# Kernel tuning notes

Measured on AMD Instinct MI355X. Metric: run time of the kernel, lower is better.

## Reference

```python
import jax, jax.numpy as jnp
import numpy as np

KAPPA = 0.1          # temperature for sinkhorn routing
SINK_ITERS = 3
SINK_EPS = 1e-6
NORM_EPS = 1e-12     # F.normalize clamp
LOG_EPS = 2.220446049250313e-16  # np.finfo(float).eps
K_TOP = 1


def _l2norm(v, axis=-1):
    n = jnp.sqrt(jnp.sum(v * v, axis=axis, keepdims=True))
    return v / jnp.maximum(n, NORM_EPS)


def _sinkhorn(log_alpha):
    # log_alpha: [K, N]
    L = jnp.exp(log_alpha)
    for _ in range(SINK_ITERS):
        L = L / (jnp.sum(L, axis=1, keepdims=True) + SINK_EPS)
        L = L / (jnp.sum(L, axis=0, keepdims=True) + SINK_EPS)
    return L


def setup_inputs() -> dict:
    key = jax.random.key(0)
    ks = jax.random.split(key, 16)
    dim = 1024
    N = 32768
    lora_dim = [8, 16, 32, 48, 64, 96, 128]
    inp = {
        "x": jax.random.normal(ks[0], (N, dim), dtype=jnp.float32),
        "prototypes": jax.random.normal(ks[1], (7, dim), dtype=jnp.float32),
    }
    for e, d in enumerate(lora_dim):
        # torch Linear weight: [out_features, in_features]
        inp[f"A{e}"] = jax.random.normal(ks[2 + 2 * e], (d, dim), dtype=jnp.float32) * (1.0 / np.sqrt(dim))
        inp[f"B{e}"] = jax.random.normal(ks[3 + 2 * e], (dim, d), dtype=jnp.float32) * (1.0 / np.sqrt(d))
    return inp


def reference(x, prototypes, A0, B0, A1, B1, A2, B2, A3, B3, A4, B4, A5, B5, A6, B6):
    A = [A0, A1, A2, A3, A4, A5, A6]
    B = [B0, B1, B2, B3, B4, B5, B6]
    N = x.shape[0]
    num_experts = len(A)

    # --- sinkhorn routing: gates [N, K] ---
    x_n = _l2norm(x)                       # [N, D]
    p_n = _l2norm(prototypes)              # [K, D]
    sim = jnp.einsum('kd,nd->kn', p_n, x_n)  # [K, N]
    L = _sinkhorn(sim / KAPPA)             # [K, N] doubly-stochastic-ish
    gates_full = L.T                       # [N, K]

    # --- top-k sparsification (k=1) ---
    top_vals, top_idx = jax.lax.top_k(gates_full, K_TOP)  # [N, k]
    gates = jnp.zeros_like(gates_full).at[jnp.arange(N)[:, None], top_idx].set(top_vals)

    # --- per-expert LoRA + weighted log-space combine ---
    # combine: out[b] = log( sum_e gates[b,e] * exp(B_e(A_e(x_b))) ), eps floor
    combined = jnp.zeros_like(x)
    for e in range(num_experts):
        y = jnp.einsum('nr,dr->nd', jnp.einsum('nd,rd->nr', x, A[e]), B[e])  # [N, D]
        combined = combined + gates[:, e:e + 1] * jnp.exp(y)
    combined = jnp.where(combined == 0, LOG_EPS, combined)
    return jnp.log(combined)
```

## Files before the change

kernel.cpp:

```cpp
#include <hip/hip_runtime.h>
#include <math.h>

#define NTOK 32768
#define DIM  1024
#define NE   7

#define PN_OFF   0
#define R1_OFF   7168
#define R2_OFF   7176
#define R3_OFF   7184
#define CNT_OFF  7192
#define PR1_OFF  7200
#define PR2_OFF  23584
#define PR3_OFF  24608
#define E0_OFF   25632
#define LG_OFF   287776
#define LIST_OFF 320544
#define A16_OFF  549920
#define B16_OFF  754720

#define SEPS 1e-6f

typedef __attribute__((ext_vector_type(8))) short short8v;
typedef __attribute__((ext_vector_type(4))) float f32x4;

constexpr int DV[7]   = {8, 16, 32, 48, 64, 96, 128};
constexpr int DPV[7]  = {32, 32, 32, 64, 64, 96, 128};
constexpr int DAPV[7] = {16, 16, 32, 48, 64, 96, 128};
constexpr int AOV[7]  = {0, 16384, 32768, 65536, 114688, 180224, 278528};
constexpr int BOV[7]  = {0, 32768, 65536, 98304, 163840, 229376, 327680};

struct ExpPtrs { const float* A[NE]; const float* B[NE]; };

__device__ __forceinline__ short f2bf(float f) {
  union { float f; unsigned u; } v; v.f = f;
  return (short)((v.u + 0x7FFFu + ((v.u >> 16) & 1u)) >> 16);
}

__device__ __forceinline__ float wsum(float v) {
  #pragma unroll
  for (int off = 32; off > 0; off >>= 1) v += __shfl_xor(v, off);
  return v;
}

__device__ __forceinline__ float dot4acc(float4 a, float4 b, float acc) {
  acc = fmaf(a.x, b.x, acc);
  acc = fmaf(a.y, b.y, acc);
  acc = fmaf(a.z, b.z, acc);
  acc = fmaf(a.w, b.w, acc);
  return acc;
}

__device__ __forceinline__ void ecfg(int e, int& d, int& dp, int& dap, int& ao, int& bo) {
  switch (e) {
    case 0: d = 8;   dp = 32;  dap = 16;  ao = 0;      bo = 0;      break;
    case 1: d = 16;  dp = 32;  dap = 16;  ao = 16384;  bo = 32768;  break;
    case 2: d = 32;  dp = 32;  dap = 32;  ao = 32768;  bo = 65536;  break;
    case 3: d = 48;  dp = 64;  dap = 48;  ao = 65536;  bo = 98304;  break;
    case 4: d = 64;  dp = 64;  dap = 64;  ao = 114688; bo = 163840; break;
    case 5: d = 96;  dp = 96;  dap = 96;  ao = 180224; bo = 229376; break;
    default: d = 128; dp = 128; dap = 128; ao = 278528; bo = 327680; break;
  }
}

__global__ __launch_bounds__(256) void k_conv(ExpPtrs p, short* __restrict__ A16,
                                              short* __restrict__ B16,
                                              const float* __restrict__ proto,
                                              float* __restrict__ wsf,
                                              int* __restrict__ counts) {
  const int e = blockIdx.y;
  const int tid = threadIdx.x;
  int d, dp, dap, ao, bo;
  ecfg(e, d, dp, dap, ao, bo);

  if (blockIdx.x == 0) {
    __shared__ float pred[4];
    if (e == 0 && tid < 8) counts[tid] = 0;
    const int w = tid >> 6, lane = tid & 63;
    float v4[4], ss = 0.f;
    #pragma unroll
    for (int i = 0; i < 4; ++i) {
      v4[i] = proto[e * DIM + tid + 256 * i];
      ss = fmaf(v4[i], v4[i], ss);
    }
    ss = wsum(ss);
    if (lane == 0) pred[w] = ss;
    __syncthreads();
    float tot = ((pred[0] + pred[1]) + pred[2]) + pred[3];
    float inv = 1.f / fmaxf(sqrtf(tot), 1e-12f);
    #pragma unroll
    for (int i = 0; i < 4; ++i)
      wsf[PN_OFF + e * DIM + tid + 256 * i] = v4[i] * inv;
  }

  const float* A = p.A[e];
  const float* B = p.B[e];
  short* Ad = A16 + ao;
  short* Bd = B16 + bo;
  const int t0 = blockIdx.x * 256 + tid;
  for (int i = t0; i < dap * DIM; i += 16 * 256) {
    int row = i >> 10;
    Ad[i] = (row < d) ? f2bf(A[i]) : (short)0;
  }
  for (int i = t0; i < DIM * dp; i += 16 * 256) {
    int j = i / dp, r = i - j * dp;
    Bd[i] = (r < d) ? f2bf(B[j * d + r]) : (short)0;
  }
}

__global__ __launch_bounds__(256) void k_sim(const float* __restrict__ x,
                                             const float* __restrict__ wsf,
                                             float* __restrict__ e0,
                                             float* __restrict__ pr1) {
  const int tid = threadIdx.x, w = tid >> 6, lane = tid & 63;
  const float4* pn4 = (const float4*)(wsf + PN_OFF);
  const int gw = blockIdx.x * 4 + w;
  float r1a[NE] = {0.f, 0.f, 0.f, 0.f, 0.f, 0.f, 0.f};
  for (int it = 0; it < 4; ++it) {
    const int n = gw + 8192 * it;
    const float4* xr4 = (const float4*)(x + (size_t)n * DIM);
    float xx = 0.f;
    float dk[NE] = {0.f, 0.f, 0.f, 0.f, 0.f, 0.f, 0.f};
    #pragma unroll
    for (int i = 0; i < 4; ++i) {
      float4 xv = xr4[lane + 64 * i];
      xx = dot4acc(xv, xv, xx);
      #pragma unroll
      for (int k = 0; k < NE; ++k)
        dk[k] = dot4acc(xv, pn4[k * 256 + lane + 64 * i], dk[k]);
    }
    xx = wsum(xx);
    #pragma unroll
    for (int k = 0; k < NE; ++k) dk[k] = wsum(dk[k]);
    if (lane == 0) {
      float nrm = fmaxf(sqrtf(xx), 1e-12f);
      #pragma unroll
      for (int k = 0; k < NE; ++k) {
        float ev = expf((dk[k] / nrm) / 0.1f);
        e0[(size_t)n * 8 + k] = ev;
        r1a[k] += ev;
      }
    }
  }
  __shared__ float red[4][8];
  if (lane == 0) {
    #pragma unroll
    for (int k = 0; k < NE; ++k) red[w][k] = r1a[k];
  }
  __syncthreads();
  if (tid == 0) {
    #pragma unroll
    for (int k = 0; k < NE; ++k)
      pr1[blockIdx.x * 8 + k] = ((red[0][k] + red[1][k]) + red[2][k]) + red[3][k];
  }
}

#define SUM7(l) (((((((l)[0] + (l)[1]) + (l)[2]) + (l)[3]) + (l)[4]) + (l)[5]) + (l)[6])

template<int DEPTH>
__global__ __launch_bounds__(256) void k_pass(const float* __restrict__ e0,
                                              float* __restrict__ wsf,
                                              const float* __restrict__ src, int nb,
                                              float* __restrict__ prOut,
                                              int* __restrict__ counts,
                                              int* __restrict__ list,
                                              float* __restrict__ lgv) {
  __shared__ float red2[8][33];
  __shared__ float Rcur[8];
  const int tid = threadIdx.x;
  {
    const int k = tid & 7, m = tid >> 3;
    float a = 0.f;
    for (int b = m; b < nb; b += 32) a += src[b * 8 + k];
    red2[k][m] = a;
    __syncthreads();
    if (tid < 8) {
      float s = 0.f;
      for (int mm = 0; mm < 32; ++mm) s += red2[tid][mm];
      Rcur[tid] = s;
      if (blockIdx.x == 0) {
        int roff = (DEPTH == 1) ? R1_OFF : (DEPTH == 2) ? R2_OFF : R3_OFF;
        wsf[roff + tid] = s;
      }
    }
    __syncthreads();
  }

  const int n = blockIdx.x * 256 + tid;
  float4 v0 = *(const float4*)(e0 + (size_t)n * 8);
  float4 v1 = *(const float4*)(e0 + (size_t)n * 8 + 4);
  float l[NE] = {v0.x, v0.y, v0.z, v0.w, v1.x, v1.y, v1.z};
  {
    const float* R1 = (DEPTH == 1) ? Rcur : (wsf + R1_OFF);
    #pragma unroll
    for (int k = 0; k < NE; ++k) l[k] = l[k] / (R1[k] + SEPS);
    float C = SUM7(l);
    #pragma unroll
    for (int k = 0; k < NE; ++k) l[k] = l[k] / (C + SEPS);
  }
  if constexpr (DEPTH >= 2) {
    const float* R2 = (DEPTH == 2) ? Rcur : (wsf + R2_OFF);
    #pragma unroll
    for (int k = 0; k < NE; ++k) l[k] = l[k] / (R2[k] + SEPS);
    float C = SUM7(l);
    #pragma unroll
    for (int k = 0; k < NE; ++k) l[k] = l[k] / (C + SEPS);
  }
  if constexpr (DEPTH >= 3) {
    const float* R3 = Rcur;
    #pragma unroll
    for (int k = 0; k < NE; ++k) l[k] = l[k] / (R3[k] + SEPS);
    float C = SUM7(l);
    #pragma unroll
    for (int k = 0; k < NE; ++k) l[k] = l[k] / (C + SEPS);
  }
  if constexpr (DEPTH == 3) {
    float best = l[0]; int be = 0;
    #pragma unroll
    for (int k = 1; k < NE; ++k) {
      if (l[k] > best) { best = l[k]; be = k; }
    }
    __shared__ int lcnt[8];
    __shared__ int wbase[4][8];
    __shared__ int gbase[8];
    const int w = tid >> 6, lane = tid & 63;
    if (tid < 8) lcnt[tid] = 0;
    __syncthreads();
    int rank = 0;
    #pragma unroll
    for (int k = 0; k < NE; ++k) {
      unsigned long long m = __ballot(be == k);
      if (lane == 0) wbase[w][k] = m ? atomicAdd(&lcnt[k], (int)__popcll(m)) : 0;
      if (be == k) rank = (int)__popcll(m & ((1ull << lane) - 1ull));
    }
    __syncthreads();
    if (tid < 8) gbase[tid] = lcnt[tid] ? atomicAdd(&counts[tid], lcnt[tid]) : 0;
    __syncthreads();
    int pos = gbase[be] + wbase[w][be] + rank;
    list[be * NTOK + pos] = n;
    lgv[n] = logf(best);
  } else {
    __shared__ float red[NE][256];
    #pragma unroll
    for (int k = 0; k < NE; ++k) red[k][tid] = l[k];
    __syncthreads();
    for (int off = 128; off > 0; off >>= 1) {
      if (tid < off) {
        #pragma unroll
        for (int k = 0; k < NE; ++k) red[k][tid] += red[k][tid + off];
      }
      __syncthreads();
    }
    if (tid < NE) prOut[blockIdx.x * 8 + tid] = red[tid][0];
  }
}

template<int E>
__device__ void expert_mfma(const float* __restrict__ x,
                            const short* __restrict__ A16,
                            const short* __restrict__ B16,
                            const int* __restrict__ list_e,
                            const float* __restrict__ lg,
                            int cnt, int tile, float* __restrict__ out,
                            char* lds) {
  constexpr int DP = DPV[E], DAP = DAPV[E];
  constexpr int NT1 = DAP / 16;
  constexpr int KS2 = DP / 32;
  constexpr int PP  = DAP + 4;
  constexpr int SP  = DP + 8;
  float* P = (float*)lds;
  short* T = (short*)lds;

  const short* Am = A16 + AOV[E];
  const short* Bp = B16 + BOV[E];
  const int tid = threadIdx.x;
  const int w = tid >> 6, lane = tid & 63;
  const int lo = lane & 15, hi = lane >> 4;
  const int m0 = tile * 16;

  const int myTok = list_e[min(m0 + lo, cnt - 1)];
  const float* xp = x + (size_t)myTok * DIM + w * 256 + hi * 8;
  const short* ApL = Am + lo * DIM + w * 256 + hi * 8;

  f32x4 acc1[NT1];
  #pragma unroll
  for (int t = 0; t < NT1; ++t) acc1[t] = (f32x4){0.f, 0.f, 0.f, 0.f};

  float4 nx0 = *(const float4*)(xp);
  float4 nx1 = *(const float4*)(xp + 4);
  #pragma unroll
  for (int kc = 0; kc < 256; kc += 32) {
    float4 x0 = nx0, x1 = nx1;
    if (kc + 32 < 256) {
      nx0 = *(const float4*)(xp + kc + 32);
      nx1 = *(const float4*)(xp + kc + 36);
    }
    short8v af;
    af[0] = f2bf(x0.x); af[1] = f2bf(x0.y); af[2] = f2bf(x0.z); af[3] = f2bf(x0.w);
    af[4] = f2bf(x1.x); af[5] = f2bf(x1.y); af[6] = f2bf(x1.z); af[7] = f2bf(x1.w);
    #pragma unroll
    for (int t = 0; t < NT1; ++t) {
      short8v bf = *(const short8v*)(ApL + t * 16 * DIM + kc);
      acc1[t] = __builtin_amdgcn_mfma_f32_16x16x32_bf16(af, bf, acc1[t], 0, 0, 0);
    }
  }

  float* Pw = P + (w & 1) * 16 * PP;
  if (w < 2) {
    #pragma unroll
    for (int t = 0; t < NT1; ++t)
      #pragma unroll
      for (int j = 0; j < 4; ++j)
        Pw[(hi * 4 + j) * PP + t * 16 + lo] = acc1[t][j];
  }
  __syncthreads();
  if (w >= 2) {
    #pragma unroll
    for (int t = 0; t < NT1; ++t)
      #pragma unroll
      for (int j = 0; j < 4; ++j)
        Pw[(hi * 4 + j) * PP + t * 16 + lo] += acc1[t][j];
  }
  __syncthreads();
  constexpr int NITEM = (16 * DP + 255) / 256;
  float vloc[NITEM];
  #pragma unroll
  for (int it = 0; it < NITEM; ++it) {
    int i = tid + it * 256;
    float v = 0.f;
    if (i < 16 * DP) {
      int r = i / DP, c = i - r * DP;
      if (c < DAP) v = P[r * PP + c] + P[(16 + r) * PP + c];
    }
    vloc[it] = v;
  }
  __syncthreads();
  #pragma unroll
  for (int it = 0; it < NITEM; ++it) {
    int i = tid + it * 256;
    if (i < 16 * DP) {
      int r = i / DP, c = i - r * DP;
      T[r * SP + c] = f2bf(vloc[it]);
    }
  }
  __syncthreads();

  short8v tf[KS2];
  #pragma unroll
  for (int ks = 0; ks < KS2; ++ks)
    tf[ks] = *(const short8v*)(T + lo * SP + ks * 32 + hi * 8);

  float  lgvr[4];
  float* op[4];
  #pragma unroll
  for (int j = 0; j < 4; ++j) {
    int t = list_e[min(m0 + hi * 4 + j, cnt - 1)];
    lgvr[j] = lg[t];
    op[j] = out + (size_t)t * DIM + w * 256 + lo;
  }

  const short* BpL = Bp + (size_t)(w * 256 + lo) * DP + hi * 8;
  #pragma unroll 4
  for (int nt = 0; nt < 16; ++nt) {
    f32x4 acc = (f32x4){0.f, 0.f, 0.f, 0.f};
    #pragma unroll
    for (int ks = 0; ks < KS2; ++ks) {
      short8v bf = *(const short8v*)(BpL + (size_t)nt * 16 * DP + ks * 32);
      acc = __builtin_amdgcn_mfma_f32_16x16x32_bf16(tf[ks], bf, acc, 0, 0, 0);
    }
    #pragma unroll
    for (int j = 0; j < 4; ++j)
      op[j][nt * 16] = acc[j] + lgvr[j];
  }
}

__global__ __launch_bounds__(256) void k_expert(const float* __restrict__ x,
                                                const short* __restrict__ A16,
                                                const short* __restrict__ B16,
                                                const int* __restrict__ list,
                                                const float* __restrict__ lg,
                                                const int* __restrict__ counts,
                                                float* __restrict__ out) {
  __shared__ __align__(16) char lds[16896];
  int rem = blockIdx.x;
  int e = 0, cnt;
  while (true) {
    cnt = counts[e];
    int tiles = (cnt + 15) >> 4;
    if (rem < tiles) break;
    rem -= tiles;
    if (++e == NE) return;
  }
  switch (e) {
    case 0: expert_mfma<0>(x, A16, B16, list + 0 * NTOK, lg, cnt, rem, out, lds); break;
    case 1: expert_mfma<1>(x, A16, B16, list + 1 * NTOK, lg, cnt, rem, out, lds); break;
    case 2: expert_mfma<2>(x, A16, B16, list + 2 * NTOK, lg, cnt, rem, out, lds); break;
    case 3: expert_mfma<3>(x, A16, B16, list + 3 * NTOK, lg, cnt, rem, out, lds); break;
    case 4: expert_mfma<4>(x, A16, B16, list + 4 * NTOK, lg, cnt, rem, out, lds); break;
    case 5: expert_mfma<5>(x, A16, B16, list + 5 * NTOK, lg, cnt, rem, out, lds); break;
    case 6: expert_mfma<6>(x, A16, B16, list + 6 * NTOK, lg, cnt, rem, out, lds); break;
  }
}

extern "C" void kernel_launch(void* const* d_in, const int* in_sizes, int n_in,
                              void* d_out, int out_size, void* d_ws, size_t ws_size,
                              hipStream_t stream) {
  const float* x     = (const float*)d_in[0];
  const float* proto = (const float*)d_in[1];
  ExpPtrs p;
  for (int e = 0; e < NE; ++e) {
    p.A[e] = (const float*)d_in[2 + 2 * e];
    p.B[e] = (const float*)d_in[3 + 2 * e];
  }
  float* wsf = (float*)d_ws;
  int*   wsi = (int*)d_ws;
  short* A16 = (short*)(wsf + A16_OFF);
  short* B16 = (short*)(wsf + B16_OFF);
  float* out = (float*)d_out;

  k_conv<<<dim3(16, NE), 256, 0, stream>>>(p, A16, B16, proto, wsf, wsi + CNT_OFF);
  k_sim<<<2048, 256, 0, stream>>>(x, wsf, wsf + E0_OFF, wsf + PR1_OFF);
  k_pass<1><<<128, 256, 0, stream>>>(wsf + E0_OFF, wsf, wsf + PR1_OFF, 2048,
                                     wsf + PR2_OFF, nullptr, nullptr, nullptr);
  k_pass<2><<<128, 256, 0, stream>>>(wsf + E0_OFF, wsf, wsf + PR2_OFF, 128,
                                     wsf + PR3_OFF, nullptr, nullptr, nullptr);
  k_pass<3><<<128, 256, 0, stream>>>(wsf + E0_OFF, wsf, wsf + PR3_OFF, 128,
                                     nullptr, wsi + CNT_OFF, wsi + LIST_OFF, wsf + LG_OFF);
  k_expert<<<2055, 256, 0, stream>>>(x, A16, B16, wsi + LIST_OFF,
                                     wsf + LG_OFF, wsi + CNT_OFF, out);
}
```

Baseline: 192.9 us.

## Split expert kernel into separate down-projection and up-projection kernels

The fused expert kernel is split into two launches. The first computes x·A^T per 16-token tile and stores the bf16 intermediate to a workspace buffer. The second reads it back and does the B projection plus the output write, with no LDS and higher occupancy bounds. Block indices are permuted with a stride of 1024 to interleave experts across the GPU. This trades an extra launch and a global round-trip of the small intermediate for better occupancy and load balance, and it only runs when the workspace is large enough, otherwise falling back to the fused kernel.

```diff
diff --git a/kernel.cpp b/kernel.cpp
--- a/kernel.cpp
+++ b/kernel.cpp
@@ -18,6 +18,8 @@
 #define LIST_OFF 320544
 #define A16_OFF  549920
 #define B16_OFF  754720
+#define TG_OFF_BYTES 3936384
+#define NBLK 2055
 
 #define SEPS 1e-6f
 
@@ -60,6 +62,21 @@
     case 4: d = 64;  dp = 64;  dap = 64;  ao = 114688; bo = 163840; break;
     case 5: d = 96;  dp = 96;  dap = 96;  ao = 180224; bo = 229376; break;
     default: d = 128; dp = 128; dap = 128; ao = 278528; bo = 327680; break;
+  }
+}
+
+__device__ __forceinline__ bool walk(int bid, const int* counts,
+                                     int& e, int& tile, int& cnt, int& tgoff) {
+  int rem = bid;
+  e = 0; tgoff = 0;
+  while (true) {
+    cnt = counts[e];
+    int tiles = (cnt + 15) >> 4;
+    if (rem < tiles) { tile = rem; return true; }
+    rem -= tiles;
+    int dp = (e < 3) ? 32 : (e < 5) ? 64 : (e == 5) ? 96 : 128;
+    tgoff += tiles * 16 * dp;
+    if (++e == NE) return false;
   }
 }
 
@@ -256,6 +273,161 @@
 }
 
 template<int E>
+__device__ void phA_impl(const float* __restrict__ x,
+                         const short* __restrict__ A16,
+                         const int* __restrict__ list_e,
+                         int cnt, int tile, short* __restrict__ Tt,
+                         char* lds) {
+  constexpr int DP = DPV[E], DAP = DAPV[E];
+  constexpr int NT1 = DAP / 16;
+  constexpr int PP  = DAP + 4;
+  float* P = (float*)lds;
+
+  const short* Am = A16 + AOV[E];
+  const int tid = threadIdx.x;
+  const int w = tid >> 6, lane = tid & 63;
+  const int lo = lane & 15, hi = lane >> 4;
+  const int m0 = tile * 16;
+
+  const int myTok = list_e[min(m0 + lo, cnt - 1)];
+  const float* xp = x + (size_t)myTok * DIM + w * 256 + hi * 8;
+  const short* ApL = Am + lo * DIM + w * 256 + hi * 8;
+
+  f32x4 acc1[NT1];
+  #pragma unroll
+  for (int t = 0; t < NT1; ++t) acc1[t] = (f32x4){0.f, 0.f, 0.f, 0.f};
+
+  float4 nx0 = *(const float4*)(xp);
+  float4 nx1 = *(const float4*)(xp + 4);
+  #pragma unroll
+  for (int kc = 0; kc < 256; kc += 32) {
+    float4 x0 = nx0, x1 = nx1;
+    if (kc + 32 < 256) {
+      nx0 = *(const float4*)(xp + kc + 32);
+      nx1 = *(const float4*)(xp + kc + 36);
+    }
+    short8v af;
+    af[0] = f2bf(x0.x); af[1] = f2bf(x0.y); af[2] = f2bf(x0.z); af[3] = f2bf(x0.w);
+    af[4] = f2bf(x1.x); af[5] = f2bf(x1.y); af[6] = f2bf(x1.z); af[7] = f2bf(x1.w);
+    #pragma unroll
+    for (int t = 0; t < NT1; ++t) {
+      short8v bf = *(const short8v*)(ApL + t * 16 * DIM + kc);
+      acc1[t] = __builtin_amdgcn_mfma_f32_16x16x32_bf16(af, bf, acc1[t], 0, 0, 0);
+    }
+  }
+
+  float* Pw = P + (w & 1) * 16 * PP;
+  if (w < 2) {
+    #pragma unroll
+    for (int t = 0; t < NT1; ++t)
+      #pragma unroll
+      for (int j = 0; j < 4; ++j)
+        Pw[(hi * 4 + j) * PP + t * 16 + lo] = acc1[t][j];
+  }
+  __syncthreads();
+  if (w >= 2) {
+    #pragma unroll
+    for (int t = 0; t < NT1; ++t)
+      #pragma unroll
+      for (int j = 0; j < 4; ++j)
+        Pw[(hi * 4 + j) * PP + t * 16 + lo] += acc1[t][j];
+  }
+  __syncthreads();
+  constexpr int NITEM = (16 * DP + 255) / 256;
+  #pragma unroll
+  for (int it = 0; it < NITEM; ++it) {
+    int i = tid + it * 256;
+    if (i < 16 * DP) {
+      int r = i / DP, c = i - r * DP;
+      float v = (c < DAP) ? (P[r * PP + c] + P[(16 + r) * PP + c]) : 0.f;
+      Tt[i] = f2bf(v);
+    }
+  }
+}
+
+__global__ __launch_bounds__(256, 4) void k_phA(const float* __restrict__ x,
+                                                const short* __restrict__ A16,
+                                                const int* __restrict__ list,
+                                                const int* __restrict__ counts,
+                                                short* __restrict__ TG) {
+  __shared__ __align__(16) char lds[16896];
+  int bid = ((int)blockIdx.x * 1024) % NBLK;
+  int e, tile, cnt, tgoff;
+  if (!walk(bid, counts, e, tile, cnt, tgoff)) return;
+  short* Tt;
+  switch (e) {
+    case 0: Tt = TG + tgoff + tile * 16 * DPV[0]; phA_impl<0>(x, A16, list + 0 * NTOK, cnt, tile, Tt, lds); break;
+    case 1: Tt = TG + tgoff + tile * 16 * DPV[1]; phA_impl<1>(x, A16, list + 1 * NTOK, cnt, tile, Tt, lds); break;
+    case 2: Tt = TG + tgoff + tile * 16 * DPV[2]; phA_impl<2>(x, A16, list + 2 * NTOK, cnt, tile, Tt, lds); break;
+    case 3: Tt = TG + tgoff + tile * 16 * DPV[3]; phA_impl<3>(x, A16, list + 3 * NTOK, cnt, tile, Tt, lds); break;
+    case 4: Tt = TG + tgoff + tile * 16 * DPV[4]; phA_impl<4>(x, A16, list + 4 * NTOK, cnt, tile, Tt, lds); break;
+    case 5: Tt = TG + tgoff + tile * 16 * DPV[5]; phA_impl<5>(x, A16, list + 5 * NTOK, cnt, tile, Tt, lds); break;
+    default: Tt = TG + tgoff + tile * 16 * DPV[6]; phA_impl<6>(x, A16, list + 6 * NTOK, cnt, tile, Tt, lds); break;
+  }
+}
+
+template<int E>
+__device__ void phB_impl(const short* __restrict__ Bp,
+                         const short* __restrict__ Tt,
+                         const int* __restrict__ list_e,
+                         const float* __restrict__ lg,
+                         int cnt, int tile, float* __restrict__ out) {
+  constexpr int DP = DPV[E];
+  constexpr int KS2 = DP / 32;
+  const int tid = threadIdx.x;
+  const int w = tid >> 6, lane = tid & 63;
+  const int lo = lane & 15, hi = lane >> 4;
+  const int m0 = tile * 16;
+
+  short8v tf[KS2];
+  #pragma unroll
+  for (int ks = 0; ks < KS2; ++ks)
+    tf[ks] = *(const short8v*)(Tt + lo * DP + ks * 32 + hi * 8);
+
+  int   tok[4];
+  float lgvr[4];
+  #pragma unroll
+  for (int j = 0; j < 4; ++j) {
+    tok[j] = list_e[min(m0 + hi * 4 + j, cnt - 1)];
+    lgvr[j] = lg[tok[j]];
+  }
+
+  const short* BpL = Bp + (size_t)(w * 256 + lo) * DP + hi * 8;
+  #pragma unroll 1
+  for (int nt = 0; nt < 16; ++nt) {
+    f32x4 acc = (f32x4){0.f, 0.f, 0.f, 0.f};
+    #pragma unroll
+    for (int ks = 0; ks < KS2; ++ks) {
+      short8v bf = *(const short8v*)(BpL + (size_t)nt * 16 * DP + ks * 32);
+      acc = __builtin_amdgcn_mfma_f32_16x16x32_bf16(tf[ks], bf, acc, 0, 0, 0);
+    }
+    #pragma unroll
+    for (int j = 0; j < 4; ++j)
+      out[(size_t)tok[j] * DIM + w * 256 + nt * 16 + lo] = acc[j] + lgvr[j];
+  }
+}
+
+__global__ __launch_bounds__(256, 8) void k_phB(const short* __restrict__ B16,
+                                                const short* __restrict__ TG,
+                                                const int* __restrict__ list,
+                                                const float* __restrict__ lg,
+                                                const int* __restrict__ counts,
+                                                float* __restrict__ out) {
+  int bid = ((int)blockIdx.x * 1024) % NBLK;
+  int e, tile, cnt, tgoff;
+  if (!walk(bid, counts, e, tile, cnt, tgoff)) return;
+  switch (e) {
+    case 0: phB_impl<0>(B16 + BOV[0], TG + tgoff + tile * 16 * DPV[0], list + 0 * NTOK, lg, cnt, tile, out); break;
+    case 1: phB_impl<1>(B16 + BOV[1], TG + tgoff + tile * 16 * DPV[1], list + 1 * NTOK, lg, cnt, tile, out); break;
+    case 2: phB_impl<2>(B16 + BOV[2], TG + tgoff + tile * 16 * DPV[2], list + 2 * NTOK, lg, cnt, tile, out); break;
+    case 3: phB_impl<3>(B16 + BOV[3], TG + tgoff + tile * 16 * DPV[3], list + 3 * NTOK, lg, cnt, tile, out); break;
+    case 4: phB_impl<4>(B16 + BOV[4], TG + tgoff + tile * 16 * DPV[4], list + 4 * NTOK, lg, cnt, tile, out); break;
+    case 5: phB_impl<5>(B16 + BOV[5], TG + tgoff + tile * 16 * DPV[5], list + 5 * NTOK, lg, cnt, tile, out); break;
+    default: phB_impl<6>(B16 + BOV[6], TG + tgoff + tile * 16 * DPV[6], list + 6 * NTOK, lg, cnt, tile, out); break;
+  }
+}
+
+template<int E>
 __device__ void expert_mfma(const float* __restrict__ x,
                             const short* __restrict__ A16,
                             const short* __restrict__ B16,
@@ -382,23 +554,16 @@
                                                 const int* __restrict__ counts,
                                                 float* __restrict__ out) {
   __shared__ __align__(16) char lds[16896];
-  int rem = blockIdx.x;
-  int e = 0, cnt;
-  while (true) {
-    cnt = counts[e];
-    int tiles = (cnt + 15) >> 4;
-    if (rem < tiles) break;
-    rem -= tiles;
-    if (++e == NE) return;
-  }
+  int e, tile, cnt, tgoff;
+  if (!walk(blockIdx.x, counts, e, tile, cnt, tgoff)) return;
   switch (e) {
-    case 0: expert_mfma<0>(x, A16, B16, list + 0 * NTOK, lg, cnt, rem, out, lds); break;
-    case 1: expert_mfma<1>(x, A16, B16, list + 1 * NTOK, lg, cnt, rem, out, lds); break;
-    case 2: expert_mfma<2>(x, A16, B16, list + 2 * NTOK, lg, cnt, rem, out, lds); break;
-    case 3: expert_mfma<3>(x, A16, B16, list + 3 * NTOK, lg, cnt, rem, out, lds); break;
-    case 4: expert_mfma<4>(x, A16, B16, list + 4 * NTOK, lg, cnt, rem, out, lds); break;
-    case 5: expert_mfma<5>(x, A16, B16, list + 5 * NTOK, lg, cnt, rem, out, lds); break;
-    case 6: expert_mfma<6>(x, A16, B16, list + 6 * NTOK, lg, cnt, rem, out, lds); break;
+    case 0: expert_mfma<0>(x, A16, B16, list + 0 * NTOK, lg, cnt, tile, out, lds); break;
+    case 1: expert_mfma<1>(x, A16, B16, list + 1 * NTOK, lg, cnt, tile, out, lds); break;
+    case 2: expert_mfma<2>(x, A16, B16, list + 2 * NTOK, lg, cnt, tile, out, lds); break;
+    case 3: expert_mfma<3>(x, A16, B16, list + 3 * NTOK, lg, cnt, tile, out, lds); break;
+    case 4: expert_mfma<4>(x, A16, B16, list + 4 * NTOK, lg, cnt, tile, out, lds); break;
+    case 5: expert_mfma<5>(x, A16, B16, list + 5 * NTOK, lg, cnt, tile, out, lds); break;
+    case 6: expert_mfma<6>(x, A16, B16, list + 6 * NTOK, lg, cnt, tile, out, lds); break;
   }
 }
 
@@ -416,6 +581,7 @@
   int*   wsi = (int*)d_ws;
   short* A16 = (short*)(wsf + A16_OFF);
   short* B16 = (short*)(wsf + B16_OFF);
+  short* TG  = (short*)((char*)d_ws + TG_OFF_BYTES);
   float* out = (float*)d_out;
 
   k_conv<<<dim3(16, NE), 256, 0, stream>>>(p, A16, B16, proto, wsf, wsi + CNT_OFF);
@@ -426,6 +592,12 @@
                                      wsf + PR3_OFF, nullptr, nullptr, nullptr);
   k_pass<3><<<128, 256, 0, stream>>>(wsf + E0_OFF, wsf, wsf + PR3_OFF, 128,
                                      nullptr, wsi + CNT_OFF, wsi + LIST_OFF, wsf + LG_OFF);
-  k_expert<<<2055, 256, 0, stream>>>(x, A16, B16, wsi + LIST_OFF,
-                                     wsf + LG_OFF, wsi + CNT_OFF, out);
-}
+  if (ws_size >= (size_t)TG_OFF_BYTES + 8417280u) {
+    k_phA<<<NBLK, 256, 0, stream>>>(x, A16, wsi + LIST_OFF, wsi + CNT_OFF, TG);
+    k_phB<<<NBLK, 256, 0, stream>>>(B16, TG, wsi + LIST_OFF, wsf + LG_OFF,
+                                    wsi + CNT_OFF, out);
+  } else {
+    k_expert<<<NBLK, 256, 0, stream>>>(x, A16, B16, wsi + LIST_OFF,
+                                       wsf + LG_OFF, wsi + CNT_OFF, out);
+  }
+}
```

Result: slower. 204.9 us (+6.2%).
